# Kernel tuning notes

Hardware: AMD Instinct MI355X
Metric: run time of the kernel (lower is better)

Reference implementation:

```python
import jax, jax.numpy as jnp
import numpy as np

B, V = 256, 128256


def setup_inputs() -> dict:
    key = jax.random.key(0)
    k1, k2, k3 = jax.random.split(key, 3)
    logits = jax.random.normal(k1, (B, V), dtype=jnp.float32)
    temperatures = jax.random.uniform(k2, (B,), dtype=jnp.float32, minval=0.1, maxval=1.5)
    # make a quarter of the batch greedy (temperature == 0) to exercise both paths
    temperatures = temperatures.at[::4].set(0.0)
    # uniform draws underlying the Exp(1) noise (torch: empty_like(probs).exponential_(1))
    u = jax.random.uniform(k3, (B, V), dtype=jnp.float32, minval=1e-30, maxval=1.0)
    return {"logits": logits, "temperatures": temperatures, "u": u}


def reference(logits, temperatures, u):
    logits = logits.astype(jnp.float32)
    greedy_mask = temperatures <= 1e-10                      # (B,)
    safe_t = jnp.where(greedy_mask, jnp.ones_like(temperatures), temperatures)
    scaled = logits / safe_t[:, None]                        # (B, V)
    probs = jax.nn.softmax(scaled, axis=-1)                  # (B, V)
    # Exp(1) noise from uniform draws; clamp matches torch's clamp_min_(1e-10)
    exp_noise = jnp.maximum(-jnp.log(u), 1e-10)              # (B, V)
    sample_tokens = jnp.argmax(probs / exp_noise, axis=-1)   # Gumbel-max style sampling
    greedy_tokens = jnp.argmax(logits, axis=-1)
    return jnp.where(greedy_mask, greedy_tokens, sample_tokens)
```

## Files before the change

### kernel.cpp

```cpp
#include <hip/hip_runtime.h>
#include <stdint.h>


__device__ __forceinline__ uint32_t order_f32(float f) {
    uint32_t u = __float_as_uint(f);
    return (u & 0x80000000u) ? ~u : (u | 0x80000000u);
}

__global__ __launch_bounds__(1024) void sampler_kernel(
        const float* __restrict__ logits,
        const float* __restrict__ temps,
        const float* __restrict__ u,
        int* __restrict__ out,
        int V) {
    const int row = blockIdx.x;
    const float t = temps[row];
    const bool greedy = (t <= 1e-10f);
    const float invT = greedy ? 1.0f : (1.0f / t);

    const size_t rowoff = (size_t)row * (size_t)V;
    const float4* lrow = reinterpret_cast<const float4*>(logits + rowoff);
    const float4* urow = reinterpret_cast<const float4*>(u + rowoff);
    const int nvec = V >> 2;

    float best = -__builtin_inff();
    int bidx = 0;

    if (greedy) {
        for (int i = threadIdx.x; i < nvec; i += blockDim.x) {
            float4 lg = lrow[i];
            const int base = i << 2;
            float s0 = lg.x, s1 = lg.y, s2 = lg.z, s3 = lg.w;
            if (s0 > best || (s0 == best && base + 0 < bidx)) { best = s0; bidx = base + 0; }
            if (s1 > best || (s1 == best && base + 1 < bidx)) { best = s1; bidx = base + 1; }
            if (s2 > best || (s2 == best && base + 2 < bidx)) { best = s2; bidx = base + 2; }
            if (s3 > best || (s3 == best && base + 3 < bidx)) { best = s3; bidx = base + 3; }
        }
    } else {
        for (int i = threadIdx.x; i < nvec; i += blockDim.x) {
            float4 lg = lrow[i];
            float4 uv = urow[i];
            const int base = i << 2;
            float s0 = lg.x * invT - logf(fmaxf(-logf(uv.x), 1e-10f));
            float s1 = lg.y * invT - logf(fmaxf(-logf(uv.y), 1e-10f));
            float s2 = lg.z * invT - logf(fmaxf(-logf(uv.z), 1e-10f));
            float s3 = lg.w * invT - logf(fmaxf(-logf(uv.w), 1e-10f));
            if (s0 > best || (s0 == best && base + 0 < bidx)) { best = s0; bidx = base + 0; }
            if (s1 > best || (s1 == best && base + 1 < bidx)) { best = s1; bidx = base + 1; }
            if (s2 > best || (s2 == best && base + 2 < bidx)) { best = s2; bidx = base + 2; }
            if (s3 > best || (s3 == best && base + 3 < bidx)) { best = s3; bidx = base + 3; }
        }
    }

    unsigned long long key =
        ((unsigned long long)order_f32(best) << 32) | (unsigned long long)(~(uint32_t)bidx);

    #pragma unroll
    for (int off = 32; off > 0; off >>= 1) {
        unsigned long long other = __shfl_down(key, off, 64);
        if (other > key) key = other;
    }

    __shared__ unsigned long long smax;
    if (threadIdx.x == 0) smax = 0ull;
    __syncthreads();
    if ((threadIdx.x & 63) == 0) {
        atomicMax(&smax, key);
    }
    __syncthreads();
    if (threadIdx.x == 0) {
        out[row] = (int)(~(uint32_t)(smax & 0xffffffffull));
    }
}

extern "C" void kernel_launch(void* const* d_in, const int* in_sizes, int n_in,
                              void* d_out, int out_size, void* d_ws, size_t ws_size,
                              hipStream_t stream) {
    const float* logits = (const float*)d_in[0];
    const float* temps  = (const float*)d_in[1];
    const float* u      = (const float*)d_in[2];
    int* out = (int*)d_out;

    const int B = in_sizes[1];
    const int V = in_sizes[0] / B;

    sampler_kernel<<<B, 1024, 0, stream>>>(logits, temps, u, out, V);
}
```

Baseline: 41.76 us.

## Split each row across eight blocks with a second reduce kernel, use fast log2

Each vocabulary row is now divided into eight segments, each handled by its own 512-thread block, raising the grid from 256 to 2048 blocks. Per-segment argmax keys go to workspace, and a small second kernel reduces them into the output tokens. The sampling path also switches from logf to hardware __log2f with the scale and clamp pre-multiplied by log2(e), which cuts transcendental cost but may differ slightly in precision. The split assumes V divides evenly into eight float4-aligned chunks, and the extra launch adds a little overhead.

```diff
diff --git a/kernel.cpp b/kernel.cpp
--- a/kernel.cpp
+++ b/kernel.cpp
@@ -1,50 +1,58 @@
 #include <hip/hip_runtime.h>
 #include <stdint.h>
 
+
+#define SPLIT 8
+#define T1 512
 
 __device__ __forceinline__ uint32_t order_f32(float f) {
     uint32_t u = __float_as_uint(f);
     return (u & 0x80000000u) ? ~u : (u | 0x80000000u);
 }
 
-__global__ __launch_bounds__(1024) void sampler_kernel(
+__global__ __launch_bounds__(T1) void sampler_part_kernel(
         const float* __restrict__ logits,
         const float* __restrict__ temps,
         const float* __restrict__ u,
-        int* __restrict__ out,
+        unsigned long long* __restrict__ ws,
         int V) {
-    const int row = blockIdx.x;
+    const int bid = blockIdx.x;
+    const int row = bid >> 3;
+    const int seg = bid & (SPLIT - 1);
+    const int chunk = V / SPLIT;
+    const int nvec = chunk >> 2;
+
     const float t = temps[row];
     const bool greedy = (t <= 1e-10f);
-    const float invT = greedy ? 1.0f : (1.0f / t);
+    const float invT = greedy ? 1.0f : (1.4426950408889634f / t);
+    const float CLMP = 1.4426950408889634e-10f;
 
-    const size_t rowoff = (size_t)row * (size_t)V;
-    const float4* lrow = reinterpret_cast<const float4*>(logits + rowoff);
-    const float4* urow = reinterpret_cast<const float4*>(u + rowoff);
-    const int nvec = V >> 2;
+    const size_t segoff = (size_t)row * (size_t)V + (size_t)seg * chunk;
+    const float4* lseg = reinterpret_cast<const float4*>(logits + segoff);
+    const float4* useg = reinterpret_cast<const float4*>(u + segoff);
+    const int idx0 = seg * chunk;
 
     float best = -__builtin_inff();
     int bidx = 0;
 
     if (greedy) {
-        for (int i = threadIdx.x; i < nvec; i += blockDim.x) {
-            float4 lg = lrow[i];
-            const int base = i << 2;
-            float s0 = lg.x, s1 = lg.y, s2 = lg.z, s3 = lg.w;
-            if (s0 > best || (s0 == best && base + 0 < bidx)) { best = s0; bidx = base + 0; }
-            if (s1 > best || (s1 == best && base + 1 < bidx)) { best = s1; bidx = base + 1; }
-            if (s2 > best || (s2 == best && base + 2 < bidx)) { best = s2; bidx = base + 2; }
-            if (s3 > best || (s3 == best && base + 3 < bidx)) { best = s3; bidx = base + 3; }
+        for (int i = threadIdx.x; i < nvec; i += T1) {
+            float4 lg = lseg[i];
+            const int base = idx0 + (i << 2);
+            if (lg.x > best || (lg.x == best && base + 0 < bidx)) { best = lg.x; bidx = base + 0; }
+            if (lg.y > best || (lg.y == best && base + 1 < bidx)) { best = lg.y; bidx = base + 1; }
+            if (lg.z > best || (lg.z == best && base + 2 < bidx)) { best = lg.z; bidx = base + 2; }
+            if (lg.w > best || (lg.w == best && base + 3 < bidx)) { best = lg.w; bidx = base + 3; }
         }
     } else {
-        for (int i = threadIdx.x; i < nvec; i += blockDim.x) {
-            float4 lg = lrow[i];
-            float4 uv = urow[i];
-            const int base = i << 2;
-            float s0 = lg.x * invT - logf(fmaxf(-logf(uv.x), 1e-10f));
-            float s1 = lg.y * invT - logf(fmaxf(-logf(uv.y), 1e-10f));
-            float s2 = lg.z * invT - logf(fmaxf(-logf(uv.z), 1e-10f));
-            float s3 = lg.w * invT - logf(fmaxf(-logf(uv.w), 1e-10f));
+        for (int i = threadIdx.x; i < nvec; i += T1) {
+            float4 lg = lseg[i];
+            float4 uv = useg[i];
+            const int base = idx0 + (i << 2);
+            float s0 = lg.x * invT - __log2f(fmaxf(-__log2f(uv.x), CLMP));
+            float s1 = lg.y * invT - __log2f(fmaxf(-__log2f(uv.y), CLMP));
+            float s2 = lg.z * invT - __log2f(fmaxf(-__log2f(uv.z), CLMP));
+            float s3 = lg.w * invT - __log2f(fmaxf(-__log2f(uv.w), CLMP));
             if (s0 > best || (s0 == best && base + 0 < bidx)) { best = s0; bidx = base + 0; }
             if (s1 > best || (s1 == best && base + 1 < bidx)) { best = s1; bidx = base + 1; }
             if (s2 > best || (s2 == best && base + 2 < bidx)) { best = s2; bidx = base + 2; }
@@ -64,13 +72,22 @@
     __shared__ unsigned long long smax;
     if (threadIdx.x == 0) smax = 0ull;
     __syncthreads();
-    if ((threadIdx.x & 63) == 0) {
-        atomicMax(&smax, key);
+    if ((threadIdx.x & 63) == 0) atomicMax(&smax, key);
+    __syncthreads();
+    if (threadIdx.x == 0) ws[bid] = smax;
+}
+
+__global__ __launch_bounds__(256) void sampler_reduce_kernel(
+        const unsigned long long* __restrict__ ws,
+        int* __restrict__ out) {
+    const int row = threadIdx.x;
+    unsigned long long best = ws[row * SPLIT];
+    #pragma unroll
+    for (int s = 1; s < SPLIT; ++s) {
+        unsigned long long k = ws[row * SPLIT + s];
+        if (k > best) best = k;
     }
-    __syncthreads();
-    if (threadIdx.x == 0) {
-        out[row] = (int)(~(uint32_t)(smax & 0xffffffffull));
-    }
+    out[row] = (int)(~(uint32_t)(best & 0xffffffffull));
 }
 
 extern "C" void kernel_launch(void* const* d_in, const int* in_sizes, int n_in,
@@ -80,9 +97,11 @@
     const float* temps  = (const float*)d_in[1];
     const float* u      = (const float*)d_in[2];
     int* out = (int*)d_out;
+    unsigned long long* ws = (unsigned long long*)d_ws;
 
     const int B = in_sizes[1];
     const int V = in_sizes[0] / B;
 
-    sampler_kernel<<<B, 1024, 0, stream>>>(logits, temps, u, out, V);
+    sampler_part_kernel<<<B * SPLIT, T1, 0, stream>>>(logits, temps, u, ws, V);
+    sampler_reduce_kernel<<<1, B, 0, stream>>>(ws, out);
 }
```

Result: faster. 39.72 us (-4.9%).

## Split each row across many blocks with a second reduction kernel and fast log2

Applied to the files above, without the earlier changes.

Each row is now split into segments of 4096 elements, each handled by a 256-thread block that issues all four float4 loads per thread up front. The per-segment maxima go to workspace, and a second tiny kernel reduces them per row. This spreads 256 rows over many more blocks to fill the GPU and raise memory-level parallelism. The natural logs are replaced by fast __log2f with rescaled constants, which cuts ALU cost at a small precision risk. The extra launch and workspace round-trip add overhead, and the reduce kernel assumes B is at most 256 threads.

```diff
diff --git a/kernel.cpp b/kernel.cpp
--- a/kernel.cpp
+++ b/kernel.cpp
@@ -1,55 +1,79 @@
 #include <hip/hip_runtime.h>
 #include <stdint.h>
 
+
+#define T1 256
+#define SEGF4 1024
 
 __device__ __forceinline__ uint32_t order_f32(float f) {
     uint32_t u = __float_as_uint(f);
     return (u & 0x80000000u) ? ~u : (u | 0x80000000u);
 }
 
-__global__ __launch_bounds__(1024) void sampler_kernel(
+__device__ __forceinline__ void upd(float s, int idx, float& best, int& bidx) {
+    if (s > best || (s == best && idx < bidx)) { best = s; bidx = idx; }
+}
+
+__global__ __launch_bounds__(T1) void sampler_part_kernel(
         const float* __restrict__ logits,
         const float* __restrict__ temps,
         const float* __restrict__ u,
-        int* __restrict__ out,
-        int V) {
-    const int row = blockIdx.x;
+        unsigned long long* __restrict__ ws,
+        int V, int B) {
+    const int seg = blockIdx.x;
+    const int row = blockIdx.y;
+    const int nvec = V >> 2;
+    const int lim = nvec - 1;
+    const int tid = threadIdx.x;
+
+    const int i0 = (seg * SEGF4) + tid;
+    int ia = i0           > lim ? lim : i0;
+    int ib = i0 + T1      > lim ? lim : i0 + T1;
+    int ic = i0 + 2 * T1  > lim ? lim : i0 + 2 * T1;
+    int id = i0 + 3 * T1  > lim ? lim : i0 + 3 * T1;
+
     const float t = temps[row];
     const bool greedy = (t <= 1e-10f);
-    const float invT = greedy ? 1.0f : (1.0f / t);
+    const float invT = greedy ? 1.0f : (1.4426950408889634f / t);
+    const float CLMP = 1.4426950408889634e-10f;
 
     const size_t rowoff = (size_t)row * (size_t)V;
     const float4* lrow = reinterpret_cast<const float4*>(logits + rowoff);
-    const float4* urow = reinterpret_cast<const float4*>(u + rowoff);
-    const int nvec = V >> 2;
 
     float best = -__builtin_inff();
-    int bidx = 0;
+    int bidx = 0x7fffffff;
 
     if (greedy) {
-        for (int i = threadIdx.x; i < nvec; i += blockDim.x) {
-            float4 lg = lrow[i];
-            const int base = i << 2;
-            float s0 = lg.x, s1 = lg.y, s2 = lg.z, s3 = lg.w;
-            if (s0 > best || (s0 == best && base + 0 < bidx)) { best = s0; bidx = base + 0; }
-            if (s1 > best || (s1 == best && base + 1 < bidx)) { best = s1; bidx = base + 1; }
-            if (s2 > best || (s2 == best && base + 2 < bidx)) { best = s2; bidx = base + 2; }
-            if (s3 > best || (s3 == best && base + 3 < bidx)) { best = s3; bidx = base + 3; }
-        }
+        float4 la = lrow[ia], lb = lrow[ib], lc = lrow[ic], ld = lrow[id];
+        upd(la.x, 4*ia+0, best, bidx); upd(la.y, 4*ia+1, best, bidx);
+        upd(la.z, 4*ia+2, best, bidx); upd(la.w, 4*ia+3, best, bidx);
+        upd(lb.x, 4*ib+0, best, bidx); upd(lb.y, 4*ib+1, best, bidx);
+        upd(lb.z, 4*ib+2, best, bidx); upd(lb.w, 4*ib+3, best, bidx);
+        upd(lc.x, 4*ic+0, best, bidx); upd(lc.y, 4*ic+1, best, bidx);
+        upd(lc.z, 4*ic+2, best, bidx); upd(lc.w, 4*ic+3, best, bidx);
+        upd(ld.x, 4*id+0, best, bidx); upd(ld.y, 4*id+1, best, bidx);
+        upd(ld.z, 4*id+2, best, bidx); upd(ld.w, 4*id+3, best, bidx);
     } else {
-        for (int i = threadIdx.x; i < nvec; i += blockDim.x) {
-            float4 lg = lrow[i];
-            float4 uv = urow[i];
-            const int base = i << 2;
-            float s0 = lg.x * invT - logf(fmaxf(-logf(uv.x), 1e-10f));
-            float s1 = lg.y * invT - logf(fmaxf(-logf(uv.y), 1e-10f));
-            float s2 = lg.z * invT - logf(fmaxf(-logf(uv.z), 1e-10f));
-            float s3 = lg.w * invT - logf(fmaxf(-logf(uv.w), 1e-10f));
-            if (s0 > best || (s0 == best && base + 0 < bidx)) { best = s0; bidx = base + 0; }
-            if (s1 > best || (s1 == best && base + 1 < bidx)) { best = s1; bidx = base + 1; }
-            if (s2 > best || (s2 == best && base + 2 < bidx)) { best = s2; bidx = base + 2; }
-            if (s3 > best || (s3 == best && base + 3 < bidx)) { best = s3; bidx = base + 3; }
-        }
+        const float4* urow = reinterpret_cast<const float4*>(u + rowoff);
+        float4 la = lrow[ia], lb = lrow[ib], lc = lrow[ic], ld = lrow[id];
+        float4 ua = urow[ia], ub = urow[ib], uc = urow[ic], ud = urow[id];
+        float s;
+        s = la.x * invT - __log2f(fmaxf(-__log2f(ua.x), CLMP)); upd(s, 4*ia+0, best, bidx);
+        s = la.y * invT - __log2f(fmaxf(-__log2f(ua.y), CLMP)); upd(s, 4*ia+1, best, bidx);
+        s = la.z * invT - __log2f(fmaxf(-__log2f(ua.z), CLMP)); upd(s, 4*ia+2, best, bidx);
+        s = la.w * invT - __log2f(fmaxf(-__log2f(ua.w), CLMP)); upd(s, 4*ia+3, best, bidx);
+        s = lb.x * invT - __log2f(fmaxf(-__log2f(ub.x), CLMP)); upd(s, 4*ib+0, best, bidx);
+        s = lb.y * invT - __log2f(fmaxf(-__log2f(ub.y), CLMP)); upd(s, 4*ib+1, best, bidx);
+        s = lb.z * invT - __log2f(fmaxf(-__log2f(ub.z), CLMP)); upd(s, 4*ib+2, best, bidx);
+        s = lb.w * invT - __log2f(fmaxf(-__log2f(ub.w), CLMP)); upd(s, 4*ib+3, best, bidx);
+        s = lc.x * invT - __log2f(fmaxf(-__log2f(uc.x), CLMP)); upd(s, 4*ic+0, best, bidx);
+        s = lc.y * invT - __log2f(fmaxf(-__log2f(uc.y), CLMP)); upd(s, 4*ic+1, best, bidx);
+        s = lc.z * invT - __log2f(fmaxf(-__log2f(uc.z), CLMP)); upd(s, 4*ic+2, best, bidx);
+        s = lc.w * invT - __log2f(fmaxf(-__log2f(uc.w), CLMP)); upd(s, 4*ic+3, best, bidx);
+        s = ld.x * invT - __log2f(fmaxf(-__log2f(ud.x), CLMP)); upd(s, 4*id+0, best, bidx);
+        s = ld.y * invT - __log2f(fmaxf(-__log2f(ud.y), CLMP)); upd(s, 4*id+1, best, bidx);
+        s = ld.z * invT - __log2f(fmaxf(-__log2f(ud.z), CLMP)); upd(s, 4*id+2, best, bidx);
+        s = ld.w * invT - __log2f(fmaxf(-__log2f(ud.w), CLMP)); upd(s, 4*id+3, best, bidx);
     }
 
     unsigned long long key =
@@ -64,13 +88,23 @@
     __shared__ unsigned long long smax;
     if (threadIdx.x == 0) smax = 0ull;
     __syncthreads();
-    if ((threadIdx.x & 63) == 0) {
-        atomicMax(&smax, key);
+    if ((threadIdx.x & 63) == 0) atomicMax(&smax, key);
+    __syncthreads();
+    if (threadIdx.x == 0) ws[(size_t)seg * B + row] = smax;
+}
+
+__global__ __launch_bounds__(256) void sampler_reduce_kernel(
+        const unsigned long long* __restrict__ ws,
+        int* __restrict__ out,
+        int nseg, int B) {
+    const int row = threadIdx.x;
+    unsigned long long best = 0ull;
+    #pragma unroll 8
+    for (int s = 0; s < nseg; ++s) {
+        unsigned long long k = ws[(size_t)s * B + row];
+        if (k > best) best = k;
     }
-    __syncthreads();
-    if (threadIdx.x == 0) {
-        out[row] = (int)(~(uint32_t)(smax & 0xffffffffull));
-    }
+    out[row] = (int)(~(uint32_t)(best & 0xffffffffull));
 }
 
 extern "C" void kernel_launch(void* const* d_in, const int* in_sizes, int n_in,
@@ -80,9 +114,14 @@
     const float* temps  = (const float*)d_in[1];
     const float* u      = (const float*)d_in[2];
     int* out = (int*)d_out;
+    unsigned long long* ws = (unsigned long long*)d_ws;
 
     const int B = in_sizes[1];
     const int V = in_sizes[0] / B;
+    const int nvec = V >> 2;
+    const int nseg = (nvec + SEGF4 - 1) / SEGF4;
 
-    sampler_kernel<<<B, 1024, 0, stream>>>(logits, temps, u, out, V);
+    dim3 grid(nseg, B);
+    sampler_part_kernel<<<grid, T1, 0, stream>>>(logits, temps, u, ws, V, B);
+    sampler_reduce_kernel<<<1, B, 0, stream>>>(ws, out, nseg, B);
 }
```

Result: no change. 41.86 us (+0.2%).
